# Kernel optimization log

Hardware: AMD Instinct MI355X
Metric: run time of the kernel (lower is better)

## Reference

```python
import jax, jax.numpy as jnp
import numpy as np

B, G, D, H = 8, 32, 768, 12
N = G * G
HD = D // H  # 64


def _make_rope(grid_size, head_dim):
    half = head_dim // 2
    inv_freq = 1.0 / (10000.0 ** (jnp.arange(0, half, 2, dtype=jnp.float32) / half))  # [half//2]
    pos = jnp.arange(grid_size, dtype=jnp.float32)[:, None] * inv_freq[None, :]       # [G, half//2]
    emb1 = jnp.concatenate([jnp.sin(pos), jnp.cos(pos)], axis=-1)                     # [G, half]
    emb_x = jnp.broadcast_to(emb1[None, :, :], (grid_size, grid_size, half))          # vary along x
    emb_y = jnp.broadcast_to(emb1[:, None, :], (grid_size, grid_size, half))          # vary along y
    emb = jnp.concatenate([emb_y, emb_x], axis=-1).reshape(grid_size * grid_size, head_dim)
    cos = jnp.cos(emb).reshape(1, grid_size * grid_size, 1, head_dim)
    sin = jnp.sin(emb).reshape(1, grid_size * grid_size, 1, head_dim)
    return cos, sin


def setup_inputs() -> dict:
    key = jax.random.key(0)
    kx, kw1, kb1, kw2, kb2 = jax.random.split(key, 5)
    x = jax.random.normal(kx, (B, N, D), dtype=jnp.float32)
    qkv_w = jax.random.normal(kw1, (3 * D, D), dtype=jnp.float32) * 0.02
    qkv_b = jax.random.normal(kb1, (3 * D,), dtype=jnp.float32) * 0.02
    proj_w = jax.random.normal(kw2, (D, D), dtype=jnp.float32) * 0.02
    proj_b = jax.random.normal(kb2, (D,), dtype=jnp.float32) * 0.02
    cos_emb, sin_emb = _make_rope(G, HD)
    return {"x": x, "qkv_w": qkv_w, "qkv_b": qkv_b, "proj_w": proj_w,
            "proj_b": proj_b, "cos_emb": cos_emb, "sin_emb": sin_emb}


def _apply_rope(t, cos, sin):
    # t: [B, N, H, HD]; cos/sin: [1, N, 1, HD]
    t1, t2 = t[..., 0::2], t[..., 1::2]
    rotated = jnp.concatenate([-t2, t1], axis=-1)
    return t * cos + rotated * sin


def reference(x, qkv_w, qkv_b, proj_w, proj_b, cos_emb, sin_emb):
    b, n, d = x.shape
    qkv = (x @ qkv_w.T + qkv_b).reshape(b, n, 3, H, HD)
    q, k, v = qkv[:, :, 0], qkv[:, :, 1], qkv[:, :, 2]  # [B, N, H, HD]
    q = _apply_rope(q, cos_emb, sin_emb)
    k = _apply_rope(k, cos_emb, sin_emb)
    scale = HD ** -0.5
    attn = jnp.einsum('bnhd,bmhd->bhnm', q, k) * scale
    attn = jax.nn.softmax(attn, axis=-1)
    out = jnp.einsum('bhnm,bmhd->bnhd', attn, v).reshape(b, n, d)
    return out @ proj_w.T + proj_b
```

## Files before the change

### kernel.cpp

```cpp
#include <hip/hip_runtime.h>
#include <stdint.h>
#include <stddef.h>

#define B_    8
#define NPOS  1024
#define DMODEL 768
#define NHEAD 12
#define HDIM  64
#define MTOK  (B_*NPOS)

typedef short bf16x8 __attribute__((ext_vector_type(8)));
typedef float f32x4  __attribute__((ext_vector_type(4)));

#if __has_builtin(__builtin_amdgcn_exp2f)
#define EXP2(x) __builtin_amdgcn_exp2f(x)
#else
#define EXP2(x) exp2f(x)
#endif

__device__ __forceinline__ unsigned short f2bs(float f) {
    unsigned int u = __builtin_bit_cast(unsigned int, f);
    u += 0x7FFFu + ((u >> 16) & 1u);
    return (unsigned short)(u >> 16);
}
__device__ __forceinline__ unsigned short f2bs_fast(float f) {
    unsigned int u = __builtin_bit_cast(unsigned int, f);
    return (unsigned short)((u + 0x8000u) >> 16);
}
__device__ __forceinline__ float bs2f(unsigned short s) {
    unsigned int u = ((unsigned int)s) << 16;
    return __builtin_bit_cast(float, u);
}

__device__ __forceinline__ void gload16(const void* g, void* l) {
    __builtin_amdgcn_global_load_lds(
        (const __attribute__((address_space(1))) unsigned int*)g,
        (__attribute__((address_space(3))) unsigned int*)l, 16, 0, 0);
}

__device__ __forceinline__ void stage_tile(const unsigned short* gbase, size_t stride_elems,
                                           int row0, int col0, char* lds, int R,
                                           int wave, int lane) {
    const int per_wave = R >> 5;
    for (int j = 0; j < per_wave; j++) {
        int i   = wave * per_wave + j;
        int row = i * 8 + (lane >> 3);
        int kb  = ((lane & 7) << 4) ^ ((row & 7) << 4);
        const char* src = (const char*)(gbase + (size_t)(row0 + row) * stride_elems + col0) + kb;
        gload16(src, lds + i * 1024);
    }
}

__device__ __forceinline__ bf16x8 read_frag(const char* lds, int row, int chunk) {
    int off = row * 128 + ((chunk << 4) ^ ((row & 7) << 4));
    return *(const bf16x8*)(lds + off);
}

__global__ void cvt_bf16_kernel(const float* __restrict__ src, unsigned short* __restrict__ dst, int n4) {
    int i = blockIdx.x * blockDim.x + threadIdx.x;
    int stride = gridDim.x * blockDim.x;
    for (; i < n4; i += stride) {
        float4 v = ((const float4*)src)[i];
        ushort4 o; o.x = f2bs(v.x); o.y = f2bs(v.y); o.z = f2bs(v.z); o.w = f2bs(v.w);
        ((ushort4*)dst)[i] = o;
    }
}

__global__ __launch_bounds__(256)
void qkv_gemm_rope(const unsigned short* __restrict__ xb, const unsigned short* __restrict__ wb,
                   const float* __restrict__ bias, const float* __restrict__ cosE,
                   const float* __restrict__ sinE,
                   unsigned short* __restrict__ qb, unsigned short* __restrict__ kbuf,
                   unsigned short* __restrict__ vt)
{
    __shared__ char smem[65536];
    char* As0 = smem;
    char* Bs0 = smem + 16384;
    char* As1 = smem + 32768;
    char* Bs1 = smem + 49152;
    float* ct = (float*)smem;

    const int tid = threadIdx.x;
    const int lane = tid & 63, w = tid >> 6;
    const int wr = w >> 1, wc = w & 1;

    const int bid = blockIdx.x;
    const int xcd = bid & 7, idx = bid >> 3;
    const int n0 = (idx % 18) * 128;
    const int m0 = (xcd * 8 + idx / 18) * 128;

    f32x4 acc[4][4];
    #pragma unroll
    for (int i = 0; i < 4; i++)
        #pragma unroll
        for (int j = 0; j < 4; j++) acc[i][j] = (f32x4){0.f, 0.f, 0.f, 0.f};

    stage_tile(xb, DMODEL, m0, 0, As0, 128, w, lane);
    stage_tile(wb, DMODEL, n0, 0, Bs0, 128, w, lane);
    __syncthreads();

    auto gbody = [&](int k0, char* Ac, char* Bc, char* An, char* Bn) {
        if (k0 + 64 < DMODEL) {
            stage_tile(xb, DMODEL, m0, k0 + 64, An, 128, w, lane);
            stage_tile(wb, DMODEL, n0, k0 + 64, Bn, 128, w, lane);
        }
        #pragma unroll
        for (int kc = 0; kc < 2; kc++) {
            int chunk = kc * 4 + (lane >> 4);
            bf16x8 af[4], bfr[4];
            #pragma unroll
            for (int mf = 0; mf < 4; mf++) af[mf] = read_frag(Ac, wr*64 + mf*16 + (lane & 15), chunk);
            #pragma unroll
            for (int nf = 0; nf < 4; nf++) bfr[nf] = read_frag(Bc, wc*64 + nf*16 + (lane & 15), chunk);
            #pragma unroll
            for (int mf = 0; mf < 4; mf++)
                #pragma unroll
                for (int nf = 0; nf < 4; nf++)
                    acc[mf][nf] = __builtin_amdgcn_mfma_f32_16x16x32_bf16(af[mf], bfr[nf], acc[mf][nf], 0, 0, 0);
        }
        __syncthreads();
    };

    for (int k0 = 0; k0 < DMODEL; k0 += 128) {
        gbody(k0,      As0, Bs0, As1, Bs1);
        gbody(k0 + 64, As1, Bs1, As0, Bs0);
    }

    const int s  = n0 / DMODEL;
    const int h2 = (n0 % DMODEL) / 64;
    #pragma unroll
    for (int p = 0; p < 2; p++) {
        if (wr == p) {
            #pragma unroll
            for (int mf = 0; mf < 4; mf++)
                #pragma unroll
                for (int nf = 0; nf < 4; nf++) {
                    int c = wc*64 + nf*16 + (lane & 15);
                    float bv = bias[n0 + c];
                    #pragma unroll
                    for (int reg = 0; reg < 4; reg++) {
                        int r = mf*16 + ((lane >> 4) << 2) + reg;
                        ct[r*130 + c] = acc[mf][nf][reg] + bv;
                    }
                }
        }
        __syncthreads();
        const int rowg = m0 + p*64;
        const int bb   = rowg >> 10;
        const int pos0 = rowg & 1023;
        if (s < 2) {
            unsigned short* dst = (s == 0) ? qb : kbuf;
            const float qs = (s == 0) ? 0.125f * 1.44269504f : 1.0f;
            const int d = tid & 63, r0 = tid >> 6;
            for (int r = r0; r < 64; r += 4) {
                int pos = pos0 + r;
                float cv = cosE[pos*64 + d] * qs, sv = sinE[pos*64 + d] * qs;
                #pragma unroll
                for (int hh = 0; hh < 2; hh++) {
                    const float* rowp = ct + r*130 + hh*64;
                    float val = rowp[d];
                    float rot = (d < 32) ? -rowp[2*d + 1] : rowp[2*d - 64];
                    dst[(((size_t)(bb*NHEAD + h2 + hh))*NPOS + pos)*64 + d] = f2bs(val*cv + rot*sv);
                }
            }
        } else {
            const int posi = tid & 63, c0 = tid >> 6;
            for (int cc = c0; cc < 128; cc += 4) {
                int hh = cc >> 6, d = cc & 63;
                vt[(((size_t)(bb*NHEAD + h2 + hh))*64 + d)*NPOS + pos0 + posi] =
                    f2bs(ct[posi*130 + cc]);
            }
        }
        __syncthreads();
    }
}

__global__ __launch_bounds__(256)
void attn_mfma(const unsigned short* __restrict__ qb, const unsigned short* __restrict__ kbuf,
               const unsigned short* __restrict__ vt,
               unsigned short* __restrict__ att)
{
    __shared__ char smem[49152];
    char* Kb0 = smem;
    char* Kb1 = smem + 8192;
    char* Vb0 = smem + 16384;
    char* Vb1 = smem + 24576;
    char* Pq  = smem + 32768;

    const int tid = threadIdx.x;
    const int lane = tid & 63, w = tid >> 6;
    char* Pw = Pq + w * 4096;

    const int bid = blockIdx.x;
    const int swz = (bid & 7) * 96 + (bid >> 3);
    const int bh = swz >> 3, qt = swz & 7;
    const int bb = bh / NHEAD, hh = bh % NHEAD;
    const int q0 = qt * 128;

    const unsigned short* qp = qb   + (size_t)bh * NPOS * 64;
    const unsigned short* kp = kbuf + (size_t)bh * NPOS * 64;
    const unsigned short* vp = vt   + (size_t)bh * 64 * NPOS;

    stage_tile(qp, 64, q0, 0, Pq, 128, w, lane);
    stage_tile(kp, 64, 0, 0, Kb0, 64, w, lane);
    stage_tile(vp, NPOS, 0, 0, Vb0, 64, w, lane);
    __syncthreads();
    bf16x8 qf[2][2];
    #pragma unroll
    for (int mf = 0; mf < 2; mf++)
        #pragma unroll
        for (int kc = 0; kc < 2; kc++)
            qf[mf][kc] = read_frag(Pq, w*32 + mf*16 + (lane & 15), kc*4 + (lane >> 4));
    __syncthreads();

    f32x4 O[2][4];
    float lpart[2][4];
    #pragma unroll
    for (int mf = 0; mf < 2; mf++)
        #pragma unroll
        for (int nd = 0; nd < 4; nd++) O[mf][nd] = (f32x4){0.f, 0.f, 0.f, 0.f};
    #pragma unroll
    for (int mf = 0; mf < 2; mf++)
        #pragma unroll
        for (int reg = 0; reg < 4; reg++) lpart[mf][reg] = 0.f;

    auto body = [&](int kt, char* Kc, char* Vc, char* Kn, char* Vn) {
        if (kt + 1 < 16) {
            stage_tile(kp, 64, (kt+1)*64, 0, Kn, 64, w, lane);
            stage_tile(vp, NPOS, 0, (kt+1)*64, Vn, 64, w, lane);
        }
        f32x4 S[2][4];
        #pragma unroll
        for (int mf = 0; mf < 2; mf++)
            #pragma unroll
            for (int nf = 0; nf < 4; nf++) S[mf][nf] = (f32x4){0.f, 0.f, 0.f, 0.f};
        #pragma unroll
        for (int kc = 0; kc < 2; kc++) {
            bf16x8 kf[4];
            #pragma unroll
            for (int nf = 0; nf < 4; nf++)
                kf[nf] = read_frag(Kc, nf*16 + (lane & 15), kc*4 + (lane >> 4));
            __builtin_amdgcn_s_setprio(1);
            #pragma unroll
            for (int mf = 0; mf < 2; mf++)
                #pragma unroll
                for (int nf = 0; nf < 4; nf++)
                    S[mf][nf] = __builtin_amdgcn_mfma_f32_16x16x32_bf16(qf[mf][kc], kf[nf], S[mf][nf], 0, 0, 0);
            __builtin_amdgcn_s_setprio(0);
        }

        #pragma unroll
        for (int mf = 0; mf < 2; mf++) {
            #pragma unroll
            for (int reg = 0; reg < 4; reg++) {
                int ql = mf*16 + ((lane >> 4) << 2) + reg;
                #pragma unroll
                for (int nf = 0; nf < 4; nf++) {
                    float pv = EXP2(S[mf][nf][reg]);
                    lpart[mf][reg] += pv;
                    int key = nf*16 + (lane & 15);
                    *(unsigned short*)(Pw + ql*128 + ((key*2) ^ ((ql & 7) << 4))) = f2bs_fast(pv);
                }
            }
        }

        #pragma unroll
        for (int kc = 0; kc < 2; kc++) {
            bf16x8 pf[2], vf[4];
            #pragma unroll
            for (int mf = 0; mf < 2; mf++)
                pf[mf] = read_frag(Pw, mf*16 + (lane & 15), kc*4 + (lane >> 4));
            #pragma unroll
            for (int nd = 0; nd < 4; nd++)
                vf[nd] = read_frag(Vc, nd*16 + (lane & 15), kc*4 + (lane >> 4));
            __builtin_amdgcn_s_setprio(1);
            #pragma unroll
            for (int mf = 0; mf < 2; mf++)
                #pragma unroll
                for (int nd = 0; nd < 4; nd++)
                    O[mf][nd] = __builtin_amdgcn_mfma_f32_16x16x32_bf16(pf[mf], vf[nd], O[mf][nd], 0, 0, 0);
            __builtin_amdgcn_s_setprio(0);
        }
        __syncthreads();
    };

    for (int kt = 0; kt < 16; kt += 2) {
        body(kt,     Kb0, Vb0, Kb1, Vb1);
        body(kt + 1, Kb1, Vb1, Kb0, Vb0);
    }

    #pragma unroll
    for (int mf = 0; mf < 2; mf++)
        #pragma unroll
        for (int reg = 0; reg < 4; reg++) {
            float l = lpart[mf][reg];
            l += __shfl_xor(l, 1);
            l += __shfl_xor(l, 2);
            l += __shfl_xor(l, 4);
            l += __shfl_xor(l, 8);
            float inv = 1.f / l;
            int qg = q0 + w*32 + mf*16 + ((lane >> 4) << 2) + reg;
            size_t rowb = ((size_t)bb * NPOS + qg) * DMODEL + hh * 64;
            #pragma unroll
            for (int nd = 0; nd < 4; nd++) {
                int d = nd*16 + (lane & 15);
                att[rowb + d] = f2bs(O[mf][nd][reg] * inv);
            }
        }
}

__global__ __launch_bounds__(256)
void proj_gemm(const unsigned short* __restrict__ a, const unsigned short* __restrict__ wgt,
               const float* __restrict__ bias, float* __restrict__ out)
{
    __shared__ char smem[65536];
    char* As0 = smem;
    char* Bs0 = smem + 16384;
    char* As1 = smem + 32768;
    char* Bs1 = smem + 49152;

    const int tid = threadIdx.x;
    const int lane = tid & 63, w = tid >> 6;
    const int wr = w >> 1, wc = w & 1;

    const int bid = blockIdx.x;
    const int xcd = bid & 7, idx = bid >> 3;
    const int n0 = (idx % 6) * 128;
    const int m0 = (xcd * 8 + idx / 6) * 128;

    f32x4 acc[4][4];
    #pragma unroll
    for (int i = 0; i < 4; i++)
        #pragma unroll
        for (int j = 0; j < 4; j++) acc[i][j] = (f32x4){0.f, 0.f, 0.f, 0.f};

    stage_tile(a,   DMODEL, m0, 0, As0, 128, w, lane);
    stage_tile(wgt, DMODEL, n0, 0, Bs0, 128, w, lane);
    __syncthreads();

    auto gbody = [&](int k0, char* Ac, char* Bc, char* An, char* Bn) {
        if (k0 + 64 < DMODEL) {
            stage_tile(a,   DMODEL, m0, k0 + 64, An, 128, w, lane);
            stage_tile(wgt, DMODEL, n0, k0 + 64, Bn, 128, w, lane);
        }
        #pragma unroll
        for (int kc = 0; kc < 2; kc++) {
            int chunk = kc * 4 + (lane >> 4);
            bf16x8 af[4], bfr[4];
            #pragma unroll
            for (int mf = 0; mf < 4; mf++) af[mf] = read_frag(Ac, wr*64 + mf*16 + (lane & 15), chunk);
            #pragma unroll
            for (int nf = 0; nf < 4; nf++) bfr[nf] = read_frag(Bc, wc*64 + nf*16 + (lane & 15), chunk);
            #pragma unroll
            for (int mf = 0; mf < 4; mf++)
                #pragma unroll
                for (int nf = 0; nf < 4; nf++)
                    acc[mf][nf] = __builtin_amdgcn_mfma_f32_16x16x32_bf16(af[mf], bfr[nf], acc[mf][nf], 0, 0, 0);
        }
        __syncthreads();
    };

    for (int k0 = 0; k0 < DMODEL; k0 += 128) {
        gbody(k0,      As0, Bs0, As1, Bs1);
        gbody(k0 + 64, As1, Bs1, As0, Bs0);
    }

    #pragma unroll
    for (int mf = 0; mf < 4; mf++)
        #pragma unroll
        for (int nf = 0; nf < 4; nf++) {
            int c = n0 + wc*64 + nf*16 + (lane & 15);
            float bv = bias[c];
            #pragma unroll
            for (int reg = 0; reg < 4; reg++) {
                int r = m0 + wr*64 + mf*16 + ((lane >> 4) << 2) + reg;
                out[(size_t)r * DMODEL + c] = acc[mf][nf][reg] + bv;
            }
        }
}

extern "C" void kernel_launch(void* const* d_in, const int* in_sizes, int n_in,
                              void* d_out, int out_size, void* d_ws, size_t ws_size,
                              hipStream_t stream)
{
    (void)in_sizes; (void)n_in; (void)out_size; (void)ws_size;
    const float* x      = (const float*)d_in[0];
    const float* qkv_w  = (const float*)d_in[1];
    const float* qkv_b  = (const float*)d_in[2];
    const float* proj_w = (const float*)d_in[3];
    const float* proj_b = (const float*)d_in[4];
    const float* cosE   = (const float*)d_in[5];
    const float* sinE   = (const float*)d_in[6];
    float* out = (float*)d_out;

    char* ws = (char*)d_ws;
    unsigned short* xb  = (unsigned short*)(ws);
    unsigned short* wb  = (unsigned short*)(ws + 12582912);
    unsigned short* pwb = (unsigned short*)(ws + 16121856);
    unsigned short* qb  = (unsigned short*)(ws + 17301504);
    unsigned short* kbf = (unsigned short*)(ws + 29884416);
    unsigned short* vtp = (unsigned short*)(ws + 42467328);
    unsigned short* att = (unsigned short*)(ws + 55050240);

    cvt_bf16_kernel<<<2048, 256, 0, stream>>>(x, xb, MTOK * DMODEL / 4);
    cvt_bf16_kernel<<<1728, 256, 0, stream>>>(qkv_w, wb, 3 * DMODEL * DMODEL / 4);
    cvt_bf16_kernel<<<576, 256, 0, stream>>>(proj_w, pwb, DMODEL * DMODEL / 4);

    qkv_gemm_rope<<<1152, 256, 0, stream>>>(xb, wb, qkv_b, cosE, sinE, qb, kbf, vtp);
    attn_mfma<<<768, 256, 0, stream>>>(qb, kbf, vtp, att);
    proj_gemm<<<384, 256, 0, stream>>>(att, pwb, proj_b, out);
}
```

Before: 136.1 us.

## Pipeline LDS staging with vmcnt waits, precompute offsets, merge conversion kernels

Reworks the GEMM and attention main loops to issue async global-to-LDS loads earlier and wait on them with explicit s_waitcnt vmcnt counts plus raw s_barrier, in place of full __syncthreads after each tile. Global source pointers and swizzled LDS fragment offsets are computed once before the loop, so per-iteration address arithmetic goes away. The three fp32-to-bf16 conversion launches become one kernel to cut launch overhead. The hand-counted vmcnt values depend on exact load counts, so any miscount could cause races.

After: 120.9 us. 1.13x faster.

```diff
diff --git a/kernel.cpp b/kernel.cpp
--- a/kernel.cpp
+++ b/kernel.cpp
@@ -32,37 +32,34 @@
     return __builtin_bit_cast(float, u);
 }
 
+template<int N> __device__ __forceinline__ void vwait() {
+    asm volatile("s_waitcnt vmcnt(%0)" :: "n"(N) : "memory");
+}
+
 __device__ __forceinline__ void gload16(const void* g, void* l) {
     __builtin_amdgcn_global_load_lds(
         (const __attribute__((address_space(1))) unsigned int*)g,
         (__attribute__((address_space(3))) unsigned int*)l, 16, 0, 0);
 }
 
-__device__ __forceinline__ void stage_tile(const unsigned short* gbase, size_t stride_elems,
-                                           int row0, int col0, char* lds, int R,
-                                           int wave, int lane) {
-    const int per_wave = R >> 5;
-    for (int j = 0; j < per_wave; j++) {
-        int i   = wave * per_wave + j;
-        int row = i * 8 + (lane >> 3);
-        int kb  = ((lane & 7) << 4) ^ ((row & 7) << 4);
-        const char* src = (const char*)(gbase + (size_t)(row0 + row) * stride_elems + col0) + kb;
-        gload16(src, lds + i * 1024);
-    }
-}
-
-__device__ __forceinline__ bf16x8 read_frag(const char* lds, int row, int chunk) {
-    int off = row * 128 + ((chunk << 4) ^ ((row & 7) << 4));
-    return *(const bf16x8*)(lds + off);
-}
-
-__global__ void cvt_bf16_kernel(const float* __restrict__ src, unsigned short* __restrict__ dst, int n4) {
+__global__ void cvt_all(const float* __restrict__ x, const float* __restrict__ w1,
+                        const float* __restrict__ w2,
+                        unsigned short* __restrict__ xb, unsigned short* __restrict__ wb,
+                        unsigned short* __restrict__ pwb)
+{
+    const int N0 = MTOK * DMODEL / 4;
+    const int N1 = 3 * DMODEL * DMODEL / 4;
+    const int N2 = DMODEL * DMODEL / 4;
     int i = blockIdx.x * blockDim.x + threadIdx.x;
     int stride = gridDim.x * blockDim.x;
-    for (; i < n4; i += stride) {
-        float4 v = ((const float4*)src)[i];
+    for (; i < N0 + N1 + N2; i += stride) {
+        const float4* s; unsigned short* d; int k;
+        if (i < N0)            { s = (const float4*)x;  d = xb;  k = i; }
+        else if (i < N0 + N1)  { s = (const float4*)w1; d = wb;  k = i - N0; }
+        else                   { s = (const float4*)w2; d = pwb; k = i - N0 - N1; }
+        float4 v = s[k];
         ushort4 o; o.x = f2bs(v.x); o.y = f2bs(v.y); o.z = f2bs(v.z); o.w = f2bs(v.w);
-        ((ushort4*)dst)[i] = o;
+        ((ushort4*)d)[k] = o;
     }
 }
 
@@ -89,42 +86,71 @@
     const int n0 = (idx % 18) * 128;
     const int m0 = (xcd * 8 + idx / 18) * 128;
 
+    const char* aS[4]; const char* bS[4]; int sDo[4];
+    #pragma unroll
+    for (int j = 0; j < 4; j++) {
+        int i   = w * 4 + j;
+        int row = i * 8 + (lane >> 3);
+        int kb  = ((lane & 7) << 4) ^ ((row & 7) << 4);
+        aS[j] = (const char*)(xb + (size_t)(m0 + row) * DMODEL) + kb;
+        bS[j] = (const char*)(wb + (size_t)(n0 + row) * DMODEL) + kb;
+        sDo[j] = i * 1024;
+    }
+    int aOf[2][4], bOf[2][4];
+    #pragma unroll
+    for (int kc = 0; kc < 2; kc++) {
+        int chunk = kc * 4 + (lane >> 4);
+        #pragma unroll
+        for (int f = 0; f < 4; f++) {
+            int ra = wr*64 + f*16 + (lane & 15);
+            aOf[kc][f] = ra*128 + ((chunk << 4) ^ ((ra & 7) << 4));
+            int rb = wc*64 + f*16 + (lane & 15);
+            bOf[kc][f] = rb*128 + ((chunk << 4) ^ ((rb & 7) << 4));
+        }
+    }
+
     f32x4 acc[4][4];
     #pragma unroll
     for (int i = 0; i < 4; i++)
         #pragma unroll
         for (int j = 0; j < 4; j++) acc[i][j] = (f32x4){0.f, 0.f, 0.f, 0.f};
 
-    stage_tile(xb, DMODEL, m0, 0, As0, 128, w, lane);
-    stage_tile(wb, DMODEL, n0, 0, Bs0, 128, w, lane);
-    __syncthreads();
-
-    auto gbody = [&](int k0, char* Ac, char* Bc, char* An, char* Bn) {
-        if (k0 + 64 < DMODEL) {
-            stage_tile(xb, DMODEL, m0, k0 + 64, An, 128, w, lane);
-            stage_tile(wb, DMODEL, n0, k0 + 64, Bn, 128, w, lane);
-        }
+    auto gcompute = [&](char* Ac, char* Bc) {
         #pragma unroll
         for (int kc = 0; kc < 2; kc++) {
-            int chunk = kc * 4 + (lane >> 4);
             bf16x8 af[4], bfr[4];
             #pragma unroll
-            for (int mf = 0; mf < 4; mf++) af[mf] = read_frag(Ac, wr*64 + mf*16 + (lane & 15), chunk);
-            #pragma unroll
-            for (int nf = 0; nf < 4; nf++) bfr[nf] = read_frag(Bc, wc*64 + nf*16 + (lane & 15), chunk);
+            for (int mf = 0; mf < 4; mf++) af[mf] = *(const bf16x8*)(Ac + aOf[kc][mf]);
+            #pragma unroll
+            for (int nf = 0; nf < 4; nf++) bfr[nf] = *(const bf16x8*)(Bc + bOf[kc][nf]);
             #pragma unroll
             for (int mf = 0; mf < 4; mf++)
                 #pragma unroll
                 for (int nf = 0; nf < 4; nf++)
                     acc[mf][nf] = __builtin_amdgcn_mfma_f32_16x16x32_bf16(af[mf], bfr[nf], acc[mf][nf], 0, 0, 0);
         }
-        __syncthreads();
     };
 
-    for (int k0 = 0; k0 < DMODEL; k0 += 128) {
-        gbody(k0,      As0, Bs0, As1, Bs1);
-        gbody(k0 + 64, As1, Bs1, As0, Bs0);
-    }
+#define QSTAGE(KOFF, AB, BB) do { \
+    _Pragma("unroll") for (int j = 0; j < 4; j++) gload16(aS[j] + (KOFF), (AB) + sDo[j]); \
+    _Pragma("unroll") for (int j = 0; j < 4; j++) gload16(bS[j] + (KOFF), (BB) + sDo[j]); \
+} while (0)
+
+    QSTAGE(0,   As0, Bs0);
+    QSTAGE(128, As1, Bs1);
+
+#define QSTEP(T, AC, BC, VM) \
+    vwait<VM>(); \
+    __builtin_amdgcn_s_barrier(); \
+    gcompute(AC, BC); \
+    __builtin_amdgcn_s_barrier(); \
+    if ((T) + 2 < 12) QSTAGE(((T) + 2) * 128, AC, BC);
+
+#define QPAIR(T, VM1) QSTEP(T, As0, Bs0, 8) QSTEP((T)+1, As1, Bs1, VM1)
+    QPAIR(0, 8) QPAIR(2, 8) QPAIR(4, 8) QPAIR(6, 8) QPAIR(8, 8) QPAIR(10, 0)
+#undef QPAIR
+#undef QSTEP
+#undef QSTAGE
 
     const int s  = n0 / DMODEL;
     const int h2 = (n0 % DMODEL) / 64;
@@ -201,17 +227,54 @@
     const unsigned short* kp = kbuf + (size_t)bh * NPOS * 64;
     const unsigned short* vp = vt   + (size_t)bh * 64 * NPOS;
 
-    stage_tile(qp, 64, q0, 0, Pq, 128, w, lane);
-    stage_tile(kp, 64, 0, 0, Kb0, 64, w, lane);
-    stage_tile(vp, NPOS, 0, 0, Vb0, 64, w, lane);
-    __syncthreads();
+    const char* kS[2]; const char* vS[2]; int kvDo[2];
+    #pragma unroll
+    for (int j = 0; j < 2; j++) {
+        int i   = w * 2 + j;
+        int row = i * 8 + (lane >> 3);
+        int kb  = ((lane & 7) << 4) ^ ((row & 7) << 4);
+        kS[j] = (const char*)(kp) + (size_t)row * 128 + kb;
+        vS[j] = (const char*)(vp) + (size_t)row * 2048 + kb;
+        kvDo[j] = i * 1024;
+    }
+    int kOf[2][4], vOf[2][4], pOf[2][2];
+    #pragma unroll
+    for (int kc = 0; kc < 2; kc++) {
+        int chunk = kc * 4 + (lane >> 4);
+        #pragma unroll
+        for (int f = 0; f < 4; f++) {
+            int r = f*16 + (lane & 15);
+            kOf[kc][f] = r*128 + ((chunk << 4) ^ ((r & 7) << 4));
+            vOf[kc][f] = kOf[kc][f];
+        }
+        #pragma unroll
+        for (int f = 0; f < 2; f++) {
+            int r = f*16 + (lane & 15);
+            pOf[kc][f] = r*128 + ((chunk << 4) ^ ((r & 7) << 4));
+        }
+    }
+
+#define ASTAGE(T, KN, VN) do { \
+    _Pragma("unroll") for (int j = 0; j < 2; j++) gload16(kS[j] + (size_t)(T) * 8192, (KN) + kvDo[j]); \
+    _Pragma("unroll") for (int j = 0; j < 2; j++) gload16(vS[j] + (T) * 128,          (VN) + kvDo[j]); \
+} while (0)
+
+    #pragma unroll
+    for (int j = 0; j < 4; j++) {
+        int i   = w * 4 + j;
+        int row = i * 8 + (lane >> 3);
+        int kb  = ((lane & 7) << 4) ^ ((row & 7) << 4);
+        gload16((const char*)(qp + (size_t)(q0 + row) * 64) + kb, Pq + i * 1024);
+    }
+    ASTAGE(0, Kb0, Vb0);
+    vwait<4>();
+    __builtin_amdgcn_s_barrier();
     bf16x8 qf[2][2];
     #pragma unroll
     for (int mf = 0; mf < 2; mf++)
         #pragma unroll
         for (int kc = 0; kc < 2; kc++)
-            qf[mf][kc] = read_frag(Pq, w*32 + mf*16 + (lane & 15), kc*4 + (lane >> 4));
-    __syncthreads();
+            qf[mf][kc] = *(const bf16x8*)(Pq + w*4096 + pOf[kc][mf]);
 
     f32x4 O[2][4];
     float lpart[2][4];
@@ -224,11 +287,7 @@
         #pragma unroll
         for (int reg = 0; reg < 4; reg++) lpart[mf][reg] = 0.f;
 
-    auto body = [&](int kt, char* Kc, char* Vc, char* Kn, char* Vn) {
-        if (kt + 1 < 16) {
-            stage_tile(kp, 64, (kt+1)*64, 0, Kn, 64, w, lane);
-            stage_tile(vp, NPOS, 0, (kt+1)*64, Vn, 64, w, lane);
-        }
+    auto abody = [&](char* Kc, char* Vc) {
         f32x4 S[2][4];
         #pragma unroll
         for (int mf = 0; mf < 2; mf++)
@@ -238,8 +297,7 @@
         for (int kc = 0; kc < 2; kc++) {
             bf16x8 kf[4];
             #pragma unroll
-            for (int nf = 0; nf < 4; nf++)
-                kf[nf] = read_frag(Kc, nf*16 + (lane & 15), kc*4 + (lane >> 4));
+            for (int nf = 0; nf < 4; nf++) kf[nf] = *(const bf16x8*)(Kc + kOf[kc][nf]);
             __builtin_amdgcn_s_setprio(1);
             #pragma unroll
             for (int mf = 0; mf < 2; mf++)
@@ -248,7 +306,6 @@
                     S[mf][nf] = __builtin_amdgcn_mfma_f32_16x16x32_bf16(qf[mf][kc], kf[nf], S[mf][nf], 0, 0, 0);
             __builtin_amdgcn_s_setprio(0);
         }
-
         #pragma unroll
         for (int mf = 0; mf < 2; mf++) {
             #pragma unroll
@@ -263,16 +320,13 @@
                 }
             }
         }
-
         #pragma unroll
         for (int kc = 0; kc < 2; kc++) {
             bf16x8 pf[2], vf[4];
             #pragma unroll
-            for (int mf = 0; mf < 2; mf++)
-                pf[mf] = read_frag(Pw, mf*16 + (lane & 15), kc*4 + (lane >> 4));
-            #pragma unroll
-            for (int nd = 0; nd < 4; nd++)
-                vf[nd] = read_frag(Vc, nd*16 + (lane & 15), kc*4 + (lane >> 4));
+            for (int mf = 0; mf < 2; mf++) pf[mf] = *(const bf16x8*)(Pw + pOf[kc][mf]);
+            #pragma unroll
+            for (int nd = 0; nd < 4; nd++) vf[nd] = *(const bf16x8*)(Vc + vOf[kc][nd]);
             __builtin_amdgcn_s_setprio(1);
             #pragma unroll
             for (int mf = 0; mf < 2; mf++)
@@ -281,13 +335,21 @@
                     O[mf][nd] = __builtin_amdgcn_mfma_f32_16x16x32_bf16(pf[mf], vf[nd], O[mf][nd], 0, 0, 0);
             __builtin_amdgcn_s_setprio(0);
         }
-        __syncthreads();
     };
 
-    for (int kt = 0; kt < 16; kt += 2) {
-        body(kt,     Kb0, Vb0, Kb1, Vb1);
-        body(kt + 1, Kb1, Vb1, Kb0, Vb0);
-    }
+#define ASTEP(T, KC, VC, KN, VN, VM) \
+    if ((T) + 1 < 16) ASTAGE((T) + 1, KN, VN); \
+    vwait<VM>(); \
+    __builtin_amdgcn_s_barrier(); \
+    abody(KC, VC); \
+    __builtin_amdgcn_s_barrier();
+
+#define APAIR(T, VM1) ASTEP(T, Kb0, Vb0, Kb1, Vb1, 4) ASTEP((T)+1, Kb1, Vb1, Kb0, Vb0, VM1)
+    APAIR(0, 4) APAIR(2, 4) APAIR(4, 4) APAIR(6, 4)
+    APAIR(8, 4) APAIR(10, 4) APAIR(12, 4) APAIR(14, 0)
+#undef APAIR
+#undef ASTEP
+#undef ASTAGE
 
     #pragma unroll
     for (int mf = 0; mf < 2; mf++)
@@ -328,42 +390,71 @@
     const int n0 = (idx % 6) * 128;
     const int m0 = (xcd * 8 + idx / 6) * 128;
 
+    const char* aS[4]; const char* bS[4]; int sDo[4];
+    #pragma unroll
+    for (int j = 0; j < 4; j++) {
+        int i   = w * 4 + j;
+        int row = i * 8 + (lane >> 3);
+        int kb  = ((lane & 7) << 4) ^ ((row & 7) << 4);
+        aS[j] = (const char*)(a   + (size_t)(m0 + row) * DMODEL) + kb;
+        bS[j] = (const char*)(wgt + (size_t)(n0 + row) * DMODEL) + kb;
+        sDo[j] = i * 1024;
+    }
+    int aOf[2][4], bOf[2][4];
+    #pragma unroll
+    for (int kc = 0; kc < 2; kc++) {
+        int chunk = kc * 4 + (lane >> 4);
+        #pragma unroll
+        for (int f = 0; f < 4; f++) {
+            int ra = wr*64 + f*16 + (lane & 15);
+            aOf[kc][f] = ra*128 + ((chunk << 4) ^ ((ra & 7) << 4));
+            int rb = wc*64 + f*16 + (lane & 15);
+            bOf[kc][f] = rb*128 + ((chunk << 4) ^ ((rb & 7) << 4));
+        }
+    }
+
     f32x4 acc[4][4];
     #pragma unroll
     for (int i = 0; i < 4; i++)
         #pragma unroll
         for (int j = 0; j < 4; j++) acc[i][j] = (f32x4){0.f, 0.f, 0.f, 0.f};
 
-    stage_tile(a,   DMODEL, m0, 0, As0, 128, w, lane);
-    stage_tile(wgt, DMODEL, n0, 0, Bs0, 128, w, lane);
-    __syncthreads();
-
-    auto gbody = [&](int k0, char* Ac, char* Bc, char* An, char* Bn) {
-        if (k0 + 64 < DMODEL) {
-            stage_tile(a,   DMODEL, m0, k0 + 64, An, 128, w, lane);
-            stage_tile(wgt, DMODEL, n0, k0 + 64, Bn, 128, w, lane);
-        }
+    auto gcompute = [&](char* Ac, char* Bc) {
         #pragma unroll
         for (int kc = 0; kc < 2; kc++) {
-            int chunk = kc * 4 + (lane >> 4);
             bf16x8 af[4], bfr[4];
             #pragma unroll
-            for (int mf = 0; mf < 4; mf++) af[mf] = read_frag(Ac, wr*64 + mf*16 + (lane & 15), chunk);
-            #pragma unroll
-            for (int nf = 0; nf < 4; nf++) bfr[nf] = read_frag(Bc, wc*64 + nf*16 + (lane & 15), chunk);
+            for (int mf = 0; mf < 4; mf++) af[mf] = *(const bf16x8*)(Ac + aOf[kc][mf]);
+            #pragma unroll
+            for (int nf = 0; nf < 4; nf++) bfr[nf] = *(const bf16x8*)(Bc + bOf[kc][nf]);
             #pragma unroll
             for (int mf = 0; mf < 4; mf++)
                 #pragma unroll
                 for (int nf = 0; nf < 4; nf++)
                     acc[mf][nf] = __builtin_amdgcn_mfma_f32_16x16x32_bf16(af[mf], bfr[nf], acc[mf][nf], 0, 0, 0);
         }
-        __syncthreads();
     };
 
-    for (int k0 = 0; k0 < DMODEL; k0 += 128) {
-        gbody(k0,      As0, Bs0, As1, Bs1);
-        gbody(k0 + 64, As1, Bs1, As0, Bs0);
-    }
+#define PSTAGE(KOFF, AB, BB) do { \
+    _Pragma("unroll") for (int j = 0; j < 4; j++) gload16(aS[j] + (KOFF), (AB) + sDo[j]); \
+    _Pragma("unroll") for (int j = 0; j < 4; j++) gload16(bS[j] + (KOFF), (BB) + sDo[j]); \
+} while (0)
+
+    PSTAGE(0,   As0, Bs0);
+    PSTAGE(128, As1, Bs1);
+
+#define PSTEP(T, AC, BC, VM) \
+    vwait<VM>(); \
+    __builtin_amdgcn_s_barrier(); \
+    gcompute(AC, BC); \
+    __builtin_amdgcn_s_barrier(); \
+    if ((T) + 2 < 12) PSTAGE(((T) + 2) * 128, AC, BC);
+
+#define PPAIR(T, VM1) PSTEP(T, As0, Bs0, 8) PSTEP((T)+1, As1, Bs1, VM1)
+    PPAIR(0, 8) PPAIR(2, 8) PPAIR(4, 8) PPAIR(6, 8) PPAIR(8, 8) PPAIR(10, 0)
+#undef PPAIR
+#undef PSTEP
+#undef PSTAGE
 
     #pragma unroll
     for (int mf = 0; mf < 4; mf++)
@@ -402,10 +493,7 @@
     unsigned short* vtp = (unsigned short*)(ws + 42467328);
     unsigned short* att = (unsigned short*)(ws + 55050240);
 
-    cvt_bf16_kernel<<<2048, 256, 0, stream>>>(x, xb, MTOK * DMODEL / 4);
-    cvt_bf16_kernel<<<1728, 256, 0, stream>>>(qkv_w, wb, 3 * DMODEL * DMODEL / 4);
-    cvt_bf16_kernel<<<576, 256, 0, stream>>>(proj_w, pwb, DMODEL * DMODEL / 4);
-
+    cvt_all<<<2048, 256, 0, stream>>>(x, qkv_w, proj_w, xb, wb, pwb);
     qkv_gemm_rope<<<1152, 256, 0, stream>>>(xb, wb, qkv_b, cosE, sinE, qb, kbf, vtp);
     attn_mfma<<<768, 256, 0, stream>>>(qb, kbf, vtp, att);
     proj_gemm<<<384, 256, 0, stream>>>(att, pwb, proj_b, out);
```
